# Kernel optimization log

Hardware: AMD Instinct MI355X
Metric: run time of the kernel (lower is better)

The kernel has to match this reference:

```python
import jax, jax.numpy as jnp
import numpy as np

N_NODES = 100000
N_EDGES = 1250000
D_FEAT = 64
UNITS = 64


def setup_inputs() -> dict:
    key = jax.random.key(0)
    k1, k2, k3 = jax.random.split(key, 3)
    features = jax.random.normal(k1, (N_NODES, D_FEAT), dtype=jnp.float32)
    edge_index = jax.random.randint(k2, (2, N_EDGES), 0, N_NODES, dtype=jnp.int64)
    weight = jax.random.normal(k3, (D_FEAT, UNITS), dtype=jnp.float32) * (1.0 / np.sqrt(D_FEAT))
    bias = jnp.zeros((UNITS,), dtype=jnp.float32)
    return {"features": features, "edge_index": edge_index, "weight": weight, "bias": bias}


def reference(features, edge_index, weight, bias):
    num_nodes = features.shape[0]
    row = edge_index[0]  # [E] destination rows of adjacency
    col = edge_index[1]  # [E] source columns
    ones = jnp.ones(row.shape[0], dtype=features.dtype)
    # degree_i = number of edges with row == i (sparse row-sum of all-ones adj)
    degrees = jax.ops.segment_sum(ones, row, num_segments=num_nodes)
    deg_inv_sqrt = jnp.power(degrees, -0.5)
    deg_inv_sqrt = jnp.where(jnp.isfinite(deg_inv_sqrt), deg_inv_sqrt, 0.0)
    # symmetric normalization per edge: D^{-1/2} A D^{-1/2}
    w = deg_inv_sqrt[row] * deg_inv_sqrt[col]  # [E]
    # SpMM: propagated[i] = sum_{e: row_e = i} w_e * features[col_e]
    msgs = features[col] * w[:, None]  # [E, F]
    propagated = jax.ops.segment_sum(msgs, row, num_segments=num_nodes)  # [N, F]
    h = propagated @ weight + bias
    return jax.nn.relu(h)
```

## Files before the change

kernel.cpp:

```cpp
#include <hip/hip_runtime.h>
#include <hip/hip_bf16.h>

#define DFEAT 64
#define SBSHIFT 9
#define SBROWS 512
#define CAPSHIFT 13
#define CAP 8192
#define CHUNK 4096
#define RPT 16
#define CURPAD 16

typedef __attribute__((ext_vector_type(8))) unsigned short ushort8;

static __device__ __forceinline__ unsigned short f2bf(float f) {
    __hip_bfloat16 h = __float2bfloat16(f);
    unsigned short u;
    __builtin_memcpy(&u, &h, 2);
    return u;
}


__global__ __launch_bounds__(256) void binA_kernel(
        const int* __restrict__ ei, int E,
        int* __restrict__ sbcursor, int* __restrict__ packed) {
    __shared__ int hist[256];
    __shared__ int cur[256];
    int t = threadIdx.x;
    hist[t] = 0;
    __syncthreads();

    int base = blockIdx.x * CHUNK;
    int rv[RPT];
#pragma unroll
    for (int k = 0; k < RPT; k++) {
        int idx = base + k * 256 + t;
        rv[k] = (idx < E) ? ei[idx] : -1;
        if (rv[k] >= 0) atomicAdd(&hist[rv[k] >> SBSHIFT], 1);
    }
    __syncthreads();

    int h = hist[t];
    cur[t] = (h > 0) ? atomicAdd(&sbcursor[t * CURPAD], h) : 0;
    __syncthreads();

#pragma unroll
    for (int k = 0; k < RPT; k++) {
        int idx = base + k * 256 + t;
        if (rv[k] >= 0) {
            int r = rv[k];
            int c = ei[E + idx];
            int sb = r >> SBSHIFT;
            int pos = atomicAdd(&cur[sb], 1);
            if (pos < CAP)
                packed[(sb << CAPSHIFT) + pos] = ((r & (SBROWS - 1)) << 17) | c;
        }
    }
}

__global__ __launch_bounds__(256) void binB_xw_kernel(
        const int* __restrict__ sbcursor, const int* __restrict__ packed,
        int* __restrict__ csr_col, int* __restrict__ row_beg,
        int* __restrict__ row_end, float* __restrict__ dis,
        const float* __restrict__ feat, const float* __restrict__ W,
        ushort8* __restrict__ Y, int n, int nSB) {
    __shared__ __align__(16) char smem[16384];

    if (blockIdx.x < nSB) {
        int* rcnt = (int*)smem;
        int* rcur = rcnt + SBROWS;
        int sb = blockIdx.x;
        int t = threadIdx.x;
        int cnt = min(sbcursor[sb * CURPAD], CAP);
        const int* pk = packed + ((size_t)sb << CAPSHIFT);
        for (int i = t; i < SBROWS; i += 256) rcnt[i] = 0;
        __syncthreads();
        for (int i = t; i < cnt; i += 256) atomicAdd(&rcnt[pk[i] >> 17], 1);
        __syncthreads();
        if (t < 64) {
            int v[8];
            int run = 0;
#pragma unroll
            for (int k = 0; k < 8; k++) { v[k] = run; run += rcnt[t * 8 + k]; }
            int x = run;
            for (int off = 1; off < 64; off <<= 1) {
                int y = __shfl_up(x, off);
                if (t >= off) x += y;
            }
            int excl = x - run;
#pragma unroll
            for (int k = 0; k < 8; k++) rcur[t * 8 + k] = excl + v[k];
        }
        __syncthreads();
        int rows = min(SBROWS, n - sb * SBROWS);
        for (int rl = t; rl < rows; rl += 256) {
            int beg = (sb << CAPSHIFT) + rcur[rl];
            int d = rcnt[rl];
            int r = sb * SBROWS + rl;
            row_beg[r] = beg;
            row_end[r] = beg + d;
            dis[r] = (d > 0) ? rsqrtf((float)d) : 0.0f;
        }
        __syncthreads();
        for (int i = t; i < cnt; i += 256) {
            int p = pk[i];
            int pos = atomicAdd(&rcur[p >> 17], 1);
            csr_col[(sb << CAPSHIFT) + pos] = p & 0x1FFFF;
        }
    } else {
        float4* sW = (float4*)smem;
        for (int i = threadIdx.x; i < DFEAT * 16; i += blockDim.x)
            sW[i] = ((const float4*)W)[i];
        __syncthreads();

        int bid = blockIdx.x - nSB;
        int q = threadIdx.x & 3;
        int lrow = threadIdx.x >> 2;
        int lane = threadIdx.x & 63;
        int qbase = lane & ~3;
        int row = bid * 64 + lrow;

        float4 x[4];
        if (row < n) {
            const float4* xp = (const float4*)(feat + (size_t)row * DFEAT) + q * 4;
            x[0] = xp[0]; x[1] = xp[1]; x[2] = xp[2]; x[3] = xp[3];
        } else {
            x[0] = x[1] = x[2] = x[3] = make_float4(0.f, 0.f, 0.f, 0.f);
        }

        float4 acc[4];
#pragma unroll
        for (int j = 0; j < 4; j++) acc[j] = make_float4(0.f, 0.f, 0.f, 0.f);

#pragma unroll
        for (int qp = 0; qp < 4; qp++) {
#pragma unroll
            for (int jj = 0; jj < 4; jj++) {
                float xs[4];
                xs[0] = __shfl(x[jj].x, qbase + qp);
                xs[1] = __shfl(x[jj].y, qbase + qp);
                xs[2] = __shfl(x[jj].z, qbase + qp);
                xs[3] = __shfl(x[jj].w, qbase + qp);
                int k0 = qp * 16 + jj * 4;
#pragma unroll
                for (int c = 0; c < 4; c++) {
                    const float4* wrow = &sW[(k0 + c) * 16 + q * 4];
#pragma unroll
                    for (int j = 0; j < 4; j++) {
                        float4 w = wrow[j];
                        acc[j].x = fmaf(xs[c], w.x, acc[j].x);
                        acc[j].y = fmaf(xs[c], w.y, acc[j].y);
                        acc[j].z = fmaf(xs[c], w.z, acc[j].z);
                        acc[j].w = fmaf(xs[c], w.w, acc[j].w);
                    }
                }
            }
        }

        if (row < n) {
            ushort8 o0, o1;
            o0[0] = f2bf(acc[0].x); o0[1] = f2bf(acc[0].y);
            o0[2] = f2bf(acc[0].z); o0[3] = f2bf(acc[0].w);
            o0[4] = f2bf(acc[1].x); o0[5] = f2bf(acc[1].y);
            o0[6] = f2bf(acc[1].z); o0[7] = f2bf(acc[1].w);
            o1[0] = f2bf(acc[2].x); o1[1] = f2bf(acc[2].y);
            o1[2] = f2bf(acc[2].z); o1[3] = f2bf(acc[2].w);
            o1[4] = f2bf(acc[3].x); o1[5] = f2bf(acc[3].y);
            o1[6] = f2bf(acc[3].z); o1[7] = f2bf(acc[3].w);
            ushort8* Yo = Y + (size_t)row * 8 + q * 2;
            Yo[0] = o0;
            Yo[1] = o1;
        }
    }
}

__global__ __launch_bounds__(256) void spmm_kernel(
        const int* __restrict__ row_beg, const int* __restrict__ row_end,
        const int* __restrict__ csr_col, const float* __restrict__ dis,
        const ushort8* __restrict__ Y, const float* __restrict__ bias,
        float* __restrict__ out, int n) {
    int wid = (int)(((long long)blockIdx.x * blockDim.x + threadIdx.x) >> 6);
    int lane = threadIdx.x & 63;
    int h = lane >> 4;
    int lq = lane & 15;
    int qb = h << 4;
    int row = wid * 4 + h;
    bool active = row < n;
    int s = active ? row_beg[row] : 0;
    int e = active ? row_end[row] : 0;
    int sub = lq >> 3;
    int f8 = lane & 7;
    float acc[8] = {0.f, 0.f, 0.f, 0.f, 0.f, 0.f, 0.f, 0.f};
    for (int base = s; base < e; base += 16) {
        int cnt = min(16, e - base);
        int c = 0;
        float dv = 0.f;
        if (lq < cnt) { c = csr_col[base + lq]; dv = dis[c]; }
        for (int i = 0; i < cnt; i += 2) {
            int ce = __shfl(c, qb + i + sub);
            float de = __shfl(dv, qb + i + sub);
            ushort8 y = Y[(size_t)ce * 8 + f8];
#pragma unroll
            for (int k = 0; k < 8; k++)
                acc[k] = fmaf(de, __uint_as_float(((unsigned)y[k]) << 16), acc[k]);
        }
    }
#pragma unroll
    for (int k = 0; k < 8; k++)
        acc[k] += __shfl_xor(acc[k], 8);
    if (active && sub == 0) {
        float dr = dis[row];
        float4 b0 = ((const float4*)bias)[f8 * 2];
        float4 b1 = ((const float4*)bias)[f8 * 2 + 1];
        float4 o0, o1;
        o0.x = fmaxf(fmaf(dr, acc[0], b0.x), 0.f);
        o0.y = fmaxf(fmaf(dr, acc[1], b0.y), 0.f);
        o0.z = fmaxf(fmaf(dr, acc[2], b0.z), 0.f);
        o0.w = fmaxf(fmaf(dr, acc[3], b0.w), 0.f);
        o1.x = fmaxf(fmaf(dr, acc[4], b1.x), 0.f);
        o1.y = fmaxf(fmaf(dr, acc[5], b1.y), 0.f);
        o1.z = fmaxf(fmaf(dr, acc[6], b1.z), 0.f);
        o1.w = fmaxf(fmaf(dr, acc[7], b1.w), 0.f);
        float4* op = (float4*)(out + (size_t)row * DFEAT + f8 * 8);
        op[0] = o0;
        op[1] = o1;
    }
}

extern "C" void kernel_launch(void* const* d_in, const int* in_sizes, int n_in,
                              void* d_out, int out_size, void* d_ws, size_t ws_size,
                              hipStream_t stream) {
    const float* feat = (const float*)d_in[0];
    const int*   ei   = (const int*)d_in[1];
    const float* W    = (const float*)d_in[2];
    const float* bias = (const float*)d_in[3];
    float* out = (float*)d_out;

    int n = in_sizes[0] / DFEAT;
    int E = in_sizes[1] / 2;
    int nSB = (n + SBROWS - 1) >> SBSHIFT;

    int* ws = (int*)d_ws;
    size_t o = 0;
    int*   sbcursor = ws + o; o += 256 * CURPAD;
    float* dis      = (float*)(ws + o); o += (size_t)n;
    int*   row_beg  = ws + o; o += (size_t)n;
    int*   row_end  = ws + o; o += (size_t)n;
    int*   packed   = ws + o; o += (size_t)nSB << CAPSHIFT;
    int*   csr_col  = ws + o; o += (size_t)nSB << CAPSHIFT;
    ushort8* Y      = (ushort8*)(ws + o);

    hipMemsetAsync(sbcursor, 0, 256 * CURPAD * sizeof(int), stream);

    int binABlocks = (E + CHUNK - 1) / CHUNK;
    int xwBlocks = (n + 63) / 64;
    binA_kernel<<<binABlocks, 256, 0, stream>>>(ei, E, sbcursor, packed);
    binB_xw_kernel<<<nSB + xwBlocks, 256, 0, stream>>>(
        sbcursor, packed, csr_col, row_beg, row_end, dis, feat, W, Y, n, nSB);
    spmm_kernel<<<((n + 3) / 4 + 3) / 4, 256, 0, stream>>>(
        row_beg, row_end, csr_col, dis, Y, bias, out, n);
}
```

Measured before the change: 162.1 us.

## Fuse binning, XW and SpMM into one persistent kernel with grid barriers

Replaces the three kernel launches with a single persistent kernel of 1024 blocks that runs all phases and separates them with a software grid barrier built on agent-scope atomics. XW work is split so part of it runs alongside the edge binning and the rest alongside the per-superblock CSR build, balancing load across the barrier-separated phases. The aim is to remove launch gaps and tail idling between kernels. It relies on all 1024 blocks being co-resident, since the barrier would deadlock otherwise, and it adds barrier spin cost.

```diff
diff --git a/kernel.cpp b/kernel.cpp
--- a/kernel.cpp
+++ b/kernel.cpp
@@ -9,6 +9,7 @@
 #define CHUNK 4096
 #define RPT 16
 #define CURPAD 16
+#define GRID 1024
 
 typedef __attribute__((ext_vector_type(8))) unsigned short ushort8;
 
@@ -20,16 +21,39 @@
 }
 
 
-__global__ __launch_bounds__(256) void binA_kernel(
-        const int* __restrict__ ei, int E,
-        int* __restrict__ sbcursor, int* __restrict__ packed) {
-    __shared__ int hist[256];
-    __shared__ int cur[256];
+static __device__ __forceinline__ void grid_barrier(int* bar) {
+    __syncthreads();
+    if (threadIdx.x == 0) {
+        __threadfence();
+        int g = __hip_atomic_load(&bar[1], __ATOMIC_RELAXED,
+                                  __HIP_MEMORY_SCOPE_AGENT);
+        int a = __hip_atomic_fetch_add(&bar[0], 1, __ATOMIC_ACQ_REL,
+                                       __HIP_MEMORY_SCOPE_AGENT);
+        if (a == (int)gridDim.x - 1) {
+            __hip_atomic_store(&bar[0], 0, __ATOMIC_RELAXED,
+                               __HIP_MEMORY_SCOPE_AGENT);
+            __hip_atomic_fetch_add(&bar[1], 1, __ATOMIC_ACQ_REL,
+                                   __HIP_MEMORY_SCOPE_AGENT);
+        } else {
+            while (__hip_atomic_load(&bar[1], __ATOMIC_RELAXED,
+                                     __HIP_MEMORY_SCOPE_AGENT) == g)
+                __builtin_amdgcn_s_sleep(2);
+        }
+        __threadfence();
+    }
+    __syncthreads();
+}
+
+static __device__ __forceinline__ void binA_unit(
+        int u, const int* __restrict__ ei, int E,
+        int* __restrict__ sbcursor, int* __restrict__ packed, int* sbuf) {
+    int* hist = sbuf;
+    int* cur  = sbuf + 256;
     int t = threadIdx.x;
     hist[t] = 0;
     __syncthreads();
 
-    int base = blockIdx.x * CHUNK;
+    int base = u * CHUNK;
     int rv[RPT];
 #pragma unroll
     for (int k = 0; k < RPT; k++) {
@@ -57,133 +81,123 @@
     }
 }
 
-__global__ __launch_bounds__(256) void binB_xw_kernel(
-        const int* __restrict__ sbcursor, const int* __restrict__ packed,
+static __device__ __forceinline__ void binB_unit(
+        int sb, const int* __restrict__ sbcursor, const int* __restrict__ packed,
         int* __restrict__ csr_col, int* __restrict__ row_beg,
-        int* __restrict__ row_end, float* __restrict__ dis,
-        const float* __restrict__ feat, const float* __restrict__ W,
-        ushort8* __restrict__ Y, int n, int nSB) {
-    __shared__ __align__(16) char smem[16384];
-
-    if (blockIdx.x < nSB) {
-        int* rcnt = (int*)smem;
-        int* rcur = rcnt + SBROWS;
-        int sb = blockIdx.x;
-        int t = threadIdx.x;
-        int cnt = min(sbcursor[sb * CURPAD], CAP);
-        const int* pk = packed + ((size_t)sb << CAPSHIFT);
-        for (int i = t; i < SBROWS; i += 256) rcnt[i] = 0;
-        __syncthreads();
-        for (int i = t; i < cnt; i += 256) atomicAdd(&rcnt[pk[i] >> 17], 1);
-        __syncthreads();
-        if (t < 64) {
-            int v[8];
-            int run = 0;
-#pragma unroll
-            for (int k = 0; k < 8; k++) { v[k] = run; run += rcnt[t * 8 + k]; }
-            int x = run;
-            for (int off = 1; off < 64; off <<= 1) {
-                int y = __shfl_up(x, off);
-                if (t >= off) x += y;
-            }
-            int excl = x - run;
-#pragma unroll
-            for (int k = 0; k < 8; k++) rcur[t * 8 + k] = excl + v[k];
-        }
-        __syncthreads();
-        int rows = min(SBROWS, n - sb * SBROWS);
-        for (int rl = t; rl < rows; rl += 256) {
-            int beg = (sb << CAPSHIFT) + rcur[rl];
-            int d = rcnt[rl];
-            int r = sb * SBROWS + rl;
-            row_beg[r] = beg;
-            row_end[r] = beg + d;
-            dis[r] = (d > 0) ? rsqrtf((float)d) : 0.0f;
-        }
-        __syncthreads();
-        for (int i = t; i < cnt; i += 256) {
-            int p = pk[i];
-            int pos = atomicAdd(&rcur[p >> 17], 1);
-            csr_col[(sb << CAPSHIFT) + pos] = p & 0x1FFFF;
-        }
+        int* __restrict__ row_end, float* __restrict__ dis, int n, int* sbuf) {
+    int* rcnt = sbuf;
+    int* rcur = sbuf + 512;
+    int t = threadIdx.x;
+    int cnt = min(sbcursor[sb * CURPAD], CAP);
+    const int* pk = packed + ((size_t)sb << CAPSHIFT);
+    for (int i = t; i < SBROWS; i += 256) rcnt[i] = 0;
+    __syncthreads();
+    for (int i = t; i < cnt; i += 256) atomicAdd(&rcnt[pk[i] >> 17], 1);
+    __syncthreads();
+    if (t < 64) {
+        int v[8];
+        int run = 0;
+#pragma unroll
+        for (int k = 0; k < 8; k++) { v[k] = run; run += rcnt[t * 8 + k]; }
+        int x = run;
+        for (int off = 1; off < 64; off <<= 1) {
+            int y = __shfl_up(x, off);
+            if (t >= off) x += y;
+        }
+        int excl = x - run;
+#pragma unroll
+        for (int k = 0; k < 8; k++) rcur[t * 8 + k] = excl + v[k];
+    }
+    __syncthreads();
+    int rows = min(SBROWS, n - sb * SBROWS);
+    for (int rl = t; rl < rows; rl += 256) {
+        int beg = (sb << CAPSHIFT) + rcur[rl];
+        int d = rcnt[rl];
+        int r = sb * SBROWS + rl;
+        row_beg[r] = beg;
+        row_end[r] = beg + d;
+        dis[r] = (d > 0) ? rsqrtf((float)d) : 0.0f;
+    }
+    __syncthreads();
+    for (int i = t; i < cnt; i += 256) {
+        int p = pk[i];
+        int pos = atomicAdd(&rcur[p >> 17], 1);
+        csr_col[(sb << CAPSHIFT) + pos] = p & 0x1FFFF;
+    }
+}
+
+static __device__ __forceinline__ void xw_unit(
+        int v, const float* __restrict__ feat, const float4* sW,
+        ushort8* __restrict__ Y, int n) {
+    int q = threadIdx.x & 3;
+    int lrow = threadIdx.x >> 2;
+    int lane = threadIdx.x & 63;
+    int qbase = lane & ~3;
+    int row = v * 64 + lrow;
+
+    float4 x[4];
+    if (row < n) {
+        const float4* xp = (const float4*)(feat + (size_t)row * DFEAT) + q * 4;
+        x[0] = xp[0]; x[1] = xp[1]; x[2] = xp[2]; x[3] = xp[3];
     } else {
-        float4* sW = (float4*)smem;
-        for (int i = threadIdx.x; i < DFEAT * 16; i += blockDim.x)
-            sW[i] = ((const float4*)W)[i];
-        __syncthreads();
-
-        int bid = blockIdx.x - nSB;
-        int q = threadIdx.x & 3;
-        int lrow = threadIdx.x >> 2;
-        int lane = threadIdx.x & 63;
-        int qbase = lane & ~3;
-        int row = bid * 64 + lrow;
-
-        float4 x[4];
-        if (row < n) {
-            const float4* xp = (const float4*)(feat + (size_t)row * DFEAT) + q * 4;
-            x[0] = xp[0]; x[1] = xp[1]; x[2] = xp[2]; x[3] = xp[3];
-        } else {
-            x[0] = x[1] = x[2] = x[3] = make_float4(0.f, 0.f, 0.f, 0.f);
-        }
-
-        float4 acc[4];
-#pragma unroll
-        for (int j = 0; j < 4; j++) acc[j] = make_float4(0.f, 0.f, 0.f, 0.f);
-
-#pragma unroll
-        for (int qp = 0; qp < 4; qp++) {
-#pragma unroll
-            for (int jj = 0; jj < 4; jj++) {
-                float xs[4];
-                xs[0] = __shfl(x[jj].x, qbase + qp);
-                xs[1] = __shfl(x[jj].y, qbase + qp);
-                xs[2] = __shfl(x[jj].z, qbase + qp);
-                xs[3] = __shfl(x[jj].w, qbase + qp);
-                int k0 = qp * 16 + jj * 4;
-#pragma unroll
-                for (int c = 0; c < 4; c++) {
-                    const float4* wrow = &sW[(k0 + c) * 16 + q * 4];
-#pragma unroll
-                    for (int j = 0; j < 4; j++) {
-                        float4 w = wrow[j];
-                        acc[j].x = fmaf(xs[c], w.x, acc[j].x);
-                        acc[j].y = fmaf(xs[c], w.y, acc[j].y);
-                        acc[j].z = fmaf(xs[c], w.z, acc[j].z);
-                        acc[j].w = fmaf(xs[c], w.w, acc[j].w);
-                    }
+        x[0] = x[1] = x[2] = x[3] = make_float4(0.f, 0.f, 0.f, 0.f);
+    }
+
+    float4 acc[4];
+#pragma unroll
+    for (int j = 0; j < 4; j++) acc[j] = make_float4(0.f, 0.f, 0.f, 0.f);
+
+#pragma unroll
+    for (int qp = 0; qp < 4; qp++) {
+#pragma unroll
+        for (int jj = 0; jj < 4; jj++) {
+            float xs[4];
+            xs[0] = __shfl(x[jj].x, qbase + qp);
+            xs[1] = __shfl(x[jj].y, qbase + qp);
+            xs[2] = __shfl(x[jj].z, qbase + qp);
+            xs[3] = __shfl(x[jj].w, qbase + qp);
+            int k0 = qp * 16 + jj * 4;
+#pragma unroll
+            for (int c = 0; c < 4; c++) {
+                const float4* wrow = &sW[(k0 + c) * 16 + q * 4];
+#pragma unroll
+                for (int j = 0; j < 4; j++) {
+                    float4 w = wrow[j];
+                    acc[j].x = fmaf(xs[c], w.x, acc[j].x);
+                    acc[j].y = fmaf(xs[c], w.y, acc[j].y);
+                    acc[j].z = fmaf(xs[c], w.z, acc[j].z);
+                    acc[j].w = fmaf(xs[c], w.w, acc[j].w);
                 }
             }
         }
-
-        if (row < n) {
-            ushort8 o0, o1;
-            o0[0] = f2bf(acc[0].x); o0[1] = f2bf(acc[0].y);
-            o0[2] = f2bf(acc[0].z); o0[3] = f2bf(acc[0].w);
-            o0[4] = f2bf(acc[1].x); o0[5] = f2bf(acc[1].y);
-            o0[6] = f2bf(acc[1].z); o0[7] = f2bf(acc[1].w);
-            o1[0] = f2bf(acc[2].x); o1[1] = f2bf(acc[2].y);
-            o1[2] = f2bf(acc[2].z); o1[3] = f2bf(acc[2].w);
-            o1[4] = f2bf(acc[3].x); o1[5] = f2bf(acc[3].y);
-            o1[6] = f2bf(acc[3].z); o1[7] = f2bf(acc[3].w);
-            ushort8* Yo = Y + (size_t)row * 8 + q * 2;
-            Yo[0] = o0;
-            Yo[1] = o1;
-        }
-    }
-}
-
-__global__ __launch_bounds__(256) void spmm_kernel(
-        const int* __restrict__ row_beg, const int* __restrict__ row_end,
+    }
+
+    if (row < n) {
+        ushort8 o0, o1;
+        o0[0] = f2bf(acc[0].x); o0[1] = f2bf(acc[0].y);
+        o0[2] = f2bf(acc[0].z); o0[3] = f2bf(acc[0].w);
+        o0[4] = f2bf(acc[1].x); o0[5] = f2bf(acc[1].y);
+        o0[6] = f2bf(acc[1].z); o0[7] = f2bf(acc[1].w);
+        o1[0] = f2bf(acc[2].x); o1[1] = f2bf(acc[2].y);
+        o1[2] = f2bf(acc[2].z); o1[3] = f2bf(acc[2].w);
+        o1[4] = f2bf(acc[3].x); o1[5] = f2bf(acc[3].y);
+        o1[6] = f2bf(acc[3].z); o1[7] = f2bf(acc[3].w);
+        ushort8* Yo = Y + (size_t)row * 8 + q * 2;
+        Yo[0] = o0;
+        Yo[1] = o1;
+    }
+}
+
+static __device__ __forceinline__ void spmm_quad(
+        int wq, const int* __restrict__ row_beg, const int* __restrict__ row_end,
         const int* __restrict__ csr_col, const float* __restrict__ dis,
         const ushort8* __restrict__ Y, const float* __restrict__ bias,
         float* __restrict__ out, int n) {
-    int wid = (int)(((long long)blockIdx.x * blockDim.x + threadIdx.x) >> 6);
     int lane = threadIdx.x & 63;
     int h = lane >> 4;
     int lq = lane & 15;
     int qb = h << 4;
-    int row = wid * 4 + h;
+    int row = wq * 4 + h;
     bool active = row < n;
     int s = active ? row_beg[row] : 0;
     int e = active ? row_end[row] : 0;
@@ -226,6 +240,54 @@
     }
 }
 
+__global__ __launch_bounds__(256, 4) void fused_kernel(
+        const float* __restrict__ feat, const int* __restrict__ ei,
+        const float* __restrict__ W, const float* __restrict__ bias,
+        float* __restrict__ out, int n, int E,
+        int* bar, int* __restrict__ sbcursor, int* __restrict__ packed,
+        int* __restrict__ csr_col, int* __restrict__ row_beg,
+        int* __restrict__ row_end, float* __restrict__ dis,
+        ushort8* __restrict__ Y, int nSB, int binAUnits, int xwSplit,
+        int xwUnits) {
+    __shared__ __align__(16) float4 sW[DFEAT * 16];
+    __shared__ int sbuf[1024];
+
+    for (int i = threadIdx.x; i < DFEAT * 16; i += 256)
+        sW[i] = ((const float4*)W)[i];
+    __syncthreads();
+
+    {
+        int ph = binAUnits + xwSplit;
+        for (int u = blockIdx.x; u < ph; u += gridDim.x) {
+            if (u < binAUnits)
+                binA_unit(u, ei, E, sbcursor, packed, sbuf);
+            else
+                xw_unit(u - binAUnits, feat, sW, Y, n);
+        }
+    }
+    grid_barrier(bar);
+
+    {
+        int ph = nSB + (xwUnits - xwSplit);
+        for (int u = blockIdx.x; u < ph; u += gridDim.x) {
+            if (u < nSB)
+                binB_unit(u, sbcursor, packed, csr_col, row_beg, row_end, dis,
+                          n, sbuf);
+            else
+                xw_unit(xwSplit + (u - nSB), feat, sW, Y, n);
+        }
+    }
+    grid_barrier(bar);
+
+    {
+        int gw = (int)((blockIdx.x * 256u + threadIdx.x) >> 6);
+        int nwq = (n + 3) >> 2;
+        int stride = gridDim.x << 2;
+        for (int wq = gw; wq < nwq; wq += stride)
+            spmm_quad(wq, row_beg, row_end, csr_col, dis, Y, bias, out, n);
+    }
+}
+
 extern "C" void kernel_launch(void* const* d_in, const int* in_sizes, int n_in,
                               void* d_out, int out_size, void* d_ws, size_t ws_size,
                               hipStream_t stream) {
@@ -241,6 +303,7 @@
 
     int* ws = (int*)d_ws;
     size_t o = 0;
+    int*   bar      = ws + o; o += 16;
     int*   sbcursor = ws + o; o += 256 * CURPAD;
     float* dis      = (float*)(ws + o); o += (size_t)n;
     int*   row_beg  = ws + o; o += (size_t)n;
@@ -249,13 +312,16 @@
     int*   csr_col  = ws + o; o += (size_t)nSB << CAPSHIFT;
     ushort8* Y      = (ushort8*)(ws + o);
 
-    hipMemsetAsync(sbcursor, 0, 256 * CURPAD * sizeof(int), stream);
-
-    int binABlocks = (E + CHUNK - 1) / CHUNK;
-    int xwBlocks = (n + 63) / 64;
-    binA_kernel<<<binABlocks, 256, 0, stream>>>(ei, E, sbcursor, packed);
-    binB_xw_kernel<<<nSB + xwBlocks, 256, 0, stream>>>(
-        sbcursor, packed, csr_col, row_beg, row_end, dis, feat, W, Y, n, nSB);
-    spmm_kernel<<<((n + 3) / 4 + 3) / 4, 256, 0, stream>>>(
-        row_beg, row_end, csr_col, dis, Y, bias, out, n);
-}
+    hipMemsetAsync(ws, 0, (16 + 256 * CURPAD) * sizeof(int), stream);
+
+    int binAUnits = (E + CHUNK - 1) / CHUNK;
+    int xwUnits   = (n + 63) / 64;
+    int xwSplit = xwUnits - (GRID - nSB);
+    if (xwSplit < 0) xwSplit = 0;
+    if (xwSplit > xwUnits) xwSplit = xwUnits;
+
+    fused_kernel<<<GRID, 256, 0, stream>>>(
+        feat, ei, W, bias, out, n, E,
+        bar, sbcursor, packed, csr_col, row_beg, row_end, dis, Y,
+        nSB, binAUnits, xwSplit, xwUnits);
+}
```

Result: slower. 520.8 us (+221.3%).
